# Optimization experiments

Measured on AMD Instinct MI355X. Metric: run time of the kernel, lower is better.

## Reference

```python
import jax, jax.numpy as jnp
import numpy as np

N_USERS = 100000
N_ITEMS = 50000
EMB_DIM = 64
N_EDGES = 1000000
N_HOPS = 3
EPS = 1e-12  # F.normalize default eps


def _l2_normalize(x):
    # F.normalize(x): x / max(||x||_2, eps) along dim=1
    norm = jnp.sqrt(jnp.sum(x * x, axis=1, keepdims=True))
    return x / jnp.maximum(norm, EPS)


def setup_inputs() -> dict:
    key = jax.random.key(0)
    k1, k2, k3, k4 = jax.random.split(key, 4)
    user_emb = jax.random.normal(k1, (N_USERS, EMB_DIM), dtype=jnp.float32)
    item_emb = jax.random.normal(k2, (N_ITEMS, EMB_DIM), dtype=jnp.float32)
    user_indices = jax.random.randint(k3, (N_EDGES,), 0, N_USERS, dtype=jnp.int32)
    item_indices = jax.random.randint(k4, (N_EDGES,), 0, N_ITEMS, dtype=jnp.int32)
    return {"user_emb": user_emb, "item_emb": item_emb,
            "user_indices": user_indices, "item_indices": item_indices}


def reference(user_emb, item_emb, user_indices, item_indices):
    # mess_dropout=False, node_dropout=False (deterministic reference)
    user_agg = user_emb
    item_agg = item_emb
    user_ui_emb = jnp.zeros_like(user_emb)
    item_ui_emb = jnp.zeros_like(item_emb)
    for _ in range(N_HOPS):
        # bipartite message passing: gather from opposite side, scatter_add to own side
        msg_to_users = item_agg[item_indices]            # [E, D]
        msg_to_items = user_agg[user_indices]            # [E, D]
        user_agg = jax.ops.segment_sum(msg_to_users, user_indices, num_segments=N_USERS)
        item_agg = jax.ops.segment_sum(msg_to_items, item_indices, num_segments=N_ITEMS)
        item_agg = _l2_normalize(item_agg)
        user_agg = _l2_normalize(user_agg)
        user_ui_emb = user_agg + user_ui_emb
        item_ui_emb = item_agg + item_ui_emb
    item_ui_emb = item_ui_emb + item_emb
    user_ui_emb = user_ui_emb + user_emb
    return (item_ui_emb, user_ui_emb)
```

## Files before the change

kernel.cpp:

```cpp
#include <hip/hip_runtime.h>

#define N_USERS 100000
#define N_ITEMS 50000
#define NROWS (N_USERS + N_ITEMS)
#define EMB 64
#define N_EDGES 1000000

#define SH_U 9
#define SH_I 8
#define NBUK 196
#define B1 256
#define CHUNK ((N_EDGES + B1 - 1) / B1)
#define HN (2 * NBUK * B1)
#define HTILE 4096
#define HTILES ((HN + HTILE - 1) / HTILE)
#define DBINS 64

#define UCHUNKS 3125
#define TCHUNKS 4688
#define UXCD 3
#define UPER 1042
#define IPER 313
#define GBLOCKS (8 * UPER)

typedef unsigned short u16;
typedef u16 us8 __attribute__((ext_vector_type(8)));
typedef u16 us4 __attribute__((ext_vector_type(4)));
typedef float f4 __attribute__((ext_vector_type(4)));

static __device__ __forceinline__ float bf2f(u16 h) {
    return __uint_as_float(((unsigned)h) << 16);
}
static __device__ __forceinline__ u16 f2bf(float f) {
    unsigned u = __float_as_uint(f);
    return (u16)((u + 0x7FFFu + ((u >> 16) & 1u)) >> 16);
}

static __device__ __forceinline__ int hphys(int L) {
    int sb = L >> 8;
    int blk = L & 255;
    return blk * (2 * NBUK) + sb;
}

__global__ void conv_kernel(const float* __restrict__ ua, u16* __restrict__ ub,
                            const float* __restrict__ ia, u16* __restrict__ ib) {
    const int un4 = N_USERS * EMB / 4;
    const int in4 = N_ITEMS * EMB / 4;
    int t = blockIdx.x * blockDim.x + threadIdx.x;
    const float* a; u16* b; int idx;
    if (t < un4) { a = ua; b = ub; idx = t; }
    else if (t < un4 + in4) { a = ia; b = ib; idx = t - un4; }
    else return;
    f4 v = ((const f4*)a)[idx];
    us4 w;
    w.x = f2bf(v.x); w.y = f2bf(v.y); w.z = f2bf(v.z); w.w = f2bf(v.w);
    ((us4*)b)[idx] = w;
}

__global__ void histA_kernel(const int* __restrict__ uidx, const int* __restrict__ iidx,
                             int* __restrict__ H) {
    __shared__ int hu[NBUK];
    __shared__ int hi[NBUK];
    int tid = threadIdx.x, blk = blockIdx.x;
    for (int b = tid; b < NBUK; b += 256) { hu[b] = 0; hi[b] = 0; }
    __syncthreads();
    int e0 = blk * CHUNK;
    int e1 = e0 + CHUNK; if (e1 > N_EDGES) e1 = N_EDGES;
    for (int e = e0 + tid; e < e1; e += 256) {
        atomicAdd(&hu[uidx[e] >> SH_U], 1);
        atomicAdd(&hi[iidx[e] >> SH_I], 1);
    }
    __syncthreads();
    int* Hb = H + blk * (2 * NBUK);
    for (int b = tid; b < NBUK; b += 256) {
        Hb[b] = hu[b];
        Hb[NBUK + b] = hi[b];
    }
}

__global__ void hscan_tile_kernel(const int* __restrict__ H, int* __restrict__ part) {
    int t = blockIdx.x, tid = threadIdx.x;
    int base = t * HTILE;
    int s = 0;
    for (int i = tid; i < HTILE; i += 256) {
        int L = base + i;
        if (L < HN) s += H[hphys(L)];
    }
    #pragma unroll
    for (int o = 32; o > 0; o >>= 1) s += __shfl_xor(s, o);
    __shared__ int wsum[4];
    if ((tid & 63) == 0) wsum[tid >> 6] = s;
    __syncthreads();
    if (tid == 0) part[t] = wsum[0] + wsum[1] + wsum[2] + wsum[3];
}

__global__ void hscan_write_kernel(const int* __restrict__ H, const int* __restrict__ part,
                                   int* __restrict__ HB) {
    int t = blockIdx.x, tid = threadIdx.x;
    int base = t * HTILE;

    __shared__ int lds[HTILE];
    for (int i = tid; i < HTILE; i += 256) {
        int L = base + i;
        lds[i] = (L < HN) ? H[hphys(L)] : 0;
    }
    __syncthreads();

    int pbase = 0;
    for (int p = 0; p < t; ++p) pbase += part[p];

    int tsum = 0;
    #pragma unroll
    for (int i = 0; i < 16; ++i) tsum += lds[tid * 16 + i];

    int lane = tid & 63, wid = tid >> 6;
    int x = tsum;
    #pragma unroll
    for (int o = 1; o < 64; o <<= 1) {
        int tt = __shfl_up(x, o);
        if (lane >= o) x += tt;
    }
    __shared__ int wsum[4];
    if (lane == 63) wsum[wid] = x;
    __syncthreads();
    int wbase = 0;
    for (int w = 0; w < wid; ++w) wbase += wsum[w];

    int run = pbase + wbase + x - tsum;
    #pragma unroll
    for (int i = 0; i < 16; ++i) {
        int L = base + tid * 16 + i;
        if (L < HN) HB[L] = run;
        run += lds[tid * 16 + i];
    }
}

__global__ void scatterA_kernel(const int* __restrict__ uidx, const int* __restrict__ iidx,
                                const int* __restrict__ HB, int* __restrict__ rec) {
    __shared__ int cu[NBUK];
    __shared__ int ci[NBUK];
    int tid = threadIdx.x, blk = blockIdx.x;
    for (int sb = tid; sb < 2 * NBUK; sb += 256) {
        int v = HB[sb * B1 + blk];
        if (sb < NBUK) cu[sb] = v; else ci[sb - NBUK] = v;
    }
    __syncthreads();
    int e0 = blk * CHUNK;
    int e1 = e0 + CHUNK; if (e1 > N_EDGES) e1 = N_EDGES;
    for (int e = e0 + tid; e < e1; e += 256) {
        int u = uidx[e];
        int i = iidx[e];
        int pu = atomicAdd(&cu[u >> SH_U], 1);
        rec[pu] = ((u & 511) << 16) | i;
        int pi = atomicAdd(&ci[i >> SH_I], 1);
        rec[pi] = ((i & 255) << 17) | u;
    }
}

__global__ void bucketB_kernel(const int* __restrict__ HB, const int* __restrict__ rec,
                               int* __restrict__ list, int2* __restrict__ desc) {
    int sb = blockIdx.x, tid = threadIdx.x;
    int side = (sb >= NBUK) ? 1 : 0;
    int b = sb - side * NBUK;
    int start = HB[sb * B1];
    int end = (sb == 2 * NBUK - 1) ? 2 * N_EDGES : HB[(sb + 1) * B1];
    int shift = side ? 17 : 16;
    int mask  = side ? 0x1FFFF : 0xFFFF;
    int nd    = side ? 256 : 512;
    int dbase = side ? (b << SH_I) : (b << SH_U);
    int n     = side ? N_ITEMS : N_USERS;

    __shared__ int cnt[512];
    __shared__ int scn[512];
    __shared__ int wsum[4];
    __shared__ int dh[DBINS];
    __shared__ int dsc[DBINS];
    if (tid < 256) { cnt[tid] = 0; cnt[256 + tid] = 0; }
    if (tid < DBINS) dh[tid] = 0;
    __syncthreads();

    for (int r = start + tid; r < end; r += 256)
        atomicAdd(&cnt[rec[r] >> shift], 1);
    __syncthreads();

    int a0 = cnt[2 * tid], a1 = cnt[2 * tid + 1];
    int s = a0 + a1;
    int lane = tid & 63, wid = tid >> 6;
    int x = s;
    #pragma unroll
    for (int o = 1; o < 64; o <<= 1) {
        int tt = __shfl_up(x, o);
        if (lane >= o) x += tt;
    }
    if (lane == 63) wsum[wid] = x;
    __syncthreads();
    int wbase = 0;
    for (int w = 0; w < wid; ++w) wbase += wsum[w];
    int excl = wbase + x - s;
    scn[2 * tid] = excl;
    scn[2 * tid + 1] = excl + a0;
    __syncthreads();

    for (int r = start + tid; r < end; r += 256) {
        int v = rec[r];
        int dl = v >> shift;
        int pos = atomicAdd(&scn[dl], 1);
        list[start + pos] = (v & mask) << 7;
    }
    __syncthreads();

    int nv = n - dbase; if (nv > nd) nv = nd;
    for (int dl = tid; dl < nv; dl += 256) {
        int d = cnt[dl]; if (d > DBINS - 1) d = DBINS - 1;
        atomicAdd(&dh[d], 1);
    }
    __syncthreads();
    if (tid < DBINS) {
        int v = dh[tid];
        int xx = v;
        #pragma unroll
        for (int o = 1; o < DBINS; o <<= 1) {
            int tt = __shfl_up(xx, o);
            if (tid >= o) xx += tt;
        }
        dsc[tid] = xx - v;
    }
    __syncthreads();
    if (tid < DBINS) dh[tid] = dsc[tid];
    __syncthreads();
    int pwbase = side ? (N_USERS + dbase) : dbase;
    for (int dl = tid; dl < nv; dl += 256) {
        int deg = cnt[dl];
        int d = deg; if (d > DBINS - 1) d = DBINS - 1;
        int p = atomicAdd(&dh[d], 1);
        int absBeg = start + scn[dl] - deg;
        int rid = pwbase + dl;
        desc[pwbase + p] = make_int2(absBeg, (rid << 9) | deg);
    }
}

__global__ void gather_norm_v7(const u16* __restrict__ srcU,
                               const u16* __restrict__ srcI,
                               const int* __restrict__ list,
                               const int2* __restrict__ desc,
                               u16* __restrict__ aggU, u16* __restrict__ aggI,
                               const u16* __restrict__ h0U, const u16* __restrict__ h0I,
                               const u16* __restrict__ h1U, const u16* __restrict__ h1I,
                               float* __restrict__ outU, float* __restrict__ outI,
                               const float* __restrict__ initU, const float* __restrict__ initI,
                               int final_hop) {
    int bid = blockIdx.x;
    int xcd = bid & 7;
    int idx = bid >> 3;
    int chunk;
    if (xcd < UXCD) {
        chunk = xcd * UPER + idx;
        if (chunk >= UCHUNKS) return;
    } else {
        if (idx >= IPER) return;
        chunk = UCHUNKS + (xcd - UXCD) * IPER + idx;
        if (chunk >= TCHUNKS) return;
    }

    int t = chunk * 256 + threadIdx.x;
    int lane = t & 63;
    int grp = lane >> 3, sub = lane & 7;
    int slot = (t >> 6) * 8 + grp;

    int beg = 0, deg = 0, rid = 0;
    bool valid = slot < NROWS;
    if (valid) {
        int2 d2 = desc[slot];
        beg = d2.x;
        deg = d2.y & 511;
        rid = d2.y >> 9;
    }
    bool isU = rid < N_USERS;
    int rr = isU ? rid : rid - N_USERS;

    const u16* src  = isU ? srcU : srcI;
    const char* srcB = (const char*)src;
    unsigned suboff = (unsigned)(sub << 4);
    const int* lp = list + beg;

    float acc[8] = {0.f, 0.f, 0.f, 0.f, 0.f, 0.f, 0.f, 0.f};

    int lbase = lane & 56;
    int nfull16 = deg >> 4;
    int e0 = 0;
    for (int b16 = 0; b16 < nfull16; ++b16) {
        int jba = lp[e0 + sub];
        int jbb = lp[e0 + 8 + sub];
        #pragma unroll
        for (int e = 0; e < 8; ++e) {
            unsigned jb = (unsigned)__shfl(jba, lbase | e);
            us8 v = *(const us8*)(srcB + (jb + suboff));
            #pragma unroll
            for (int i = 0; i < 8; ++i) acc[i] += bf2f(v[i]);
        }
        #pragma unroll
        for (int e = 0; e < 8; ++e) {
            unsigned jb = (unsigned)__shfl(jbb, lbase | e);
            us8 v = *(const us8*)(srcB + (jb + suboff));
            #pragma unroll
            for (int i = 0; i < 8; ++i) acc[i] += bf2f(v[i]);
        }
        e0 += 16;
    }
    if (deg & 8) {
        int jba = lp[e0 + sub];
        #pragma unroll
        for (int e = 0; e < 8; ++e) {
            unsigned jb = (unsigned)__shfl(jba, lbase | e);
            us8 v = *(const us8*)(srcB + (jb + suboff));
            #pragma unroll
            for (int i = 0; i < 8; ++i) acc[i] += bf2f(v[i]);
        }
        e0 += 8;
    }
    int rem = deg & 7;
    if (rem) {
        int jba = lp[e0 + sub];
        #pragma unroll
        for (int e = 0; e < 8; ++e) {
            if (e < rem) {
                unsigned jb = (unsigned)__shfl(jba, lbase | e);
                us8 v = *(const us8*)(srcB + (jb + suboff));
                #pragma unroll
                for (int i = 0; i < 8; ++i) acc[i] += bf2f(v[i]);
            }
        }
    }

    float q = 0.f;
    #pragma unroll
    for (int i = 0; i < 8; ++i) q += acc[i] * acc[i];
    q += __shfl_xor(q, 1);
    q += __shfl_xor(q, 2);
    q += __shfl_xor(q, 4);
    float inv = 1.f / fmaxf(sqrtf(q), 1e-12f);

    if (!valid) return;
    size_t ro = (size_t)rr * EMB + (sub << 3);

    if (!final_hop) {
        u16* agg = isU ? aggU : aggI;
        us8 w;
        #pragma unroll
        for (int i = 0; i < 8; ++i) w[i] = f2bf(acc[i] * inv);
        *(us8*)(agg + ro) = w;
    } else {
        const u16* h0 = isU ? h0U : h0I;
        const u16* h1 = isU ? h1U : h1I;
        const float* init = isU ? initU : initI;
        float* out = isU ? outU : outI;
        us8 a = *(const us8*)(h0 + ro);
        us8 b = *(const us8*)(h1 + ro);
        f4 i0 = *(const f4*)(init + ro);
        f4 i1 = *(const f4*)(init + ro + 4);
        f4 r0, r1;
        r0.x = i0.x + bf2f(a[0]) + bf2f(b[0]) + acc[0] * inv;
        r0.y = i0.y + bf2f(a[1]) + bf2f(b[1]) + acc[1] * inv;
        r0.z = i0.z + bf2f(a[2]) + bf2f(b[2]) + acc[2] * inv;
        r0.w = i0.w + bf2f(a[3]) + bf2f(b[3]) + acc[3] * inv;
        r1.x = i1.x + bf2f(a[4]) + bf2f(b[4]) + acc[4] * inv;
        r1.y = i1.y + bf2f(a[5]) + bf2f(b[5]) + acc[5] * inv;
        r1.z = i1.z + bf2f(a[6]) + bf2f(b[6]) + acc[6] * inv;
        r1.w = i1.w + bf2f(a[7]) + bf2f(b[7]) + acc[7] * inv;
        *(f4*)(out + ro)     = r0;
        *(f4*)(out + ro + 4) = r1;
    }
}

extern "C" void kernel_launch(void* const* d_in, const int* in_sizes, int n_in,
                              void* d_out, int out_size, void* d_ws, size_t ws_size,
                              hipStream_t stream) {
    const float* user_emb = (const float*)d_in[0];
    const float* item_emb = (const float*)d_in[1];
    const int*   uidx     = (const int*)d_in[2];
    const int*   iidx     = (const int*)d_in[3];

    float* out      = (float*)d_out;
    float* out_item = out;
    float* out_user = out + (size_t)N_ITEMS * EMB;

    u16* ws16    = (u16*)d_ws;
    u16* ua_bf   = ws16;
    u16* ub_bf   = ua_bf + (size_t)N_USERS * EMB;
    u16* ia_bf   = ub_bf + (size_t)N_USERS * EMB;
    u16* ib_bf   = ia_bf + (size_t)N_ITEMS * EMB;
    u16* uemb_bf = ib_bf + (size_t)N_ITEMS * EMB;
    u16* iemb_bf = uemb_bf + (size_t)N_USERS * EMB;
    int* rec     = (int*)(iemb_bf + (size_t)N_ITEMS * EMB);
    int* list    = rec + 2 * N_EDGES;
    int* H       = list + 2 * N_EDGES + 16;
    int* HB      = H + HN;
    int* part    = HB + HN;
    int2* desc   = (int2*)(part + HTILES + 1);

    conv_kernel<<<(NROWS * EMB / 4 + 255) / 256, 256, 0, stream>>>(user_emb, uemb_bf, item_emb, iemb_bf);

    histA_kernel<<<B1, 256, 0, stream>>>(uidx, iidx, H);
    hscan_tile_kernel<<<HTILES, 256, 0, stream>>>(H, part);
    hscan_write_kernel<<<HTILES, 256, 0, stream>>>(H, part, HB);
    scatterA_kernel<<<B1, 256, 0, stream>>>(uidx, iidx, HB, rec);
    bucketB_kernel<<<2 * NBUK, 256, 0, stream>>>(HB, rec, list, desc);

    gather_norm_v7<<<GBLOCKS, 256, 0, stream>>>(
        iemb_bf, uemb_bf, list, desc,
        ua_bf, ia_bf, nullptr, nullptr, nullptr, nullptr,
        nullptr, nullptr, nullptr, nullptr, 0);

    gather_norm_v7<<<GBLOCKS, 256, 0, stream>>>(
        ia_bf, ua_bf, list, desc,
        ub_bf, ib_bf, nullptr, nullptr, nullptr, nullptr,
        nullptr, nullptr, nullptr, nullptr, 0);

    gather_norm_v7<<<GBLOCKS, 256, 0, stream>>>(
        ib_bf, ub_bf, list, desc,
        nullptr, nullptr, ua_bf, ia_bf, ub_bf, ib_bf,
        out_user, out_item, user_emb, item_emb, 1);
}
```

Measured before the change: 207.0 us.

## Build CSR via chained stable counting sorts so neighbor lists are ordered

Replaces the single two-sided bucket sort with a three-pass chain of stable counting sorts: sort by item, then stably by user (producing user CSR with items in ascending order), then stably by item again (producing item CSR with users ascending). Ordered neighbor lists should make the gather kernel's embedding reads more local and improve cache hits. The cost is many more preprocessing launches and extra passes over the edge records, plus extra workspace for the intermediate streams.

```diff
diff --git a/kernel.cpp b/kernel.cpp
--- a/kernel.cpp
+++ b/kernel.cpp
@@ -11,10 +11,11 @@
 #define NBUK 196
 #define B1 256
 #define CHUNK ((N_EDGES + B1 - 1) / B1)
-#define HN (2 * NBUK * B1)
-#define HTILE 4096
-#define HTILES ((HN + HTILE - 1) / HTILE)
 #define DBINS 64
+
+#define HNS (NBUK * B1)
+#define HTILE_S 4096
+#define HTILES_S ((HNS + HTILE_S - 1) / HTILE_S)
 
 #define UCHUNKS 3125
 #define TCHUNKS 4688
@@ -24,6 +25,7 @@
 #define GBLOCKS (8 * UPER)
 
 typedef unsigned short u16;
+typedef unsigned char u8;
 typedef u16 us8 __attribute__((ext_vector_type(8)));
 typedef u16 us4 __attribute__((ext_vector_type(4)));
 typedef float f4 __attribute__((ext_vector_type(4)));
@@ -36,10 +38,10 @@
     return (u16)((u + 0x7FFFu + ((u >> 16) & 1u)) >> 16);
 }
 
-static __device__ __forceinline__ int hphys(int L) {
-    int sb = L >> 8;
+static __device__ __forceinline__ int sphys(int L) {
+    int b = L >> 8;
     int blk = L & 255;
-    return blk * (2 * NBUK) + sb;
+    return blk * NBUK + b;
 }
 
 __global__ void conv_kernel(const float* __restrict__ ua, u16* __restrict__ ub,
@@ -57,34 +59,41 @@
     ((us4*)b)[idx] = w;
 }
 
-__global__ void histA_kernel(const int* __restrict__ uidx, const int* __restrict__ iidx,
-                             int* __restrict__ H) {
-    __shared__ int hu[NBUK];
-    __shared__ int hi[NBUK];
+__global__ void histI_edges(const int* __restrict__ iidx, int* __restrict__ H) {
+    __shared__ int h[NBUK];
     int tid = threadIdx.x, blk = blockIdx.x;
-    for (int b = tid; b < NBUK; b += 256) { hu[b] = 0; hi[b] = 0; }
+    for (int b = tid; b < NBUK; b += 256) h[b] = 0;
     __syncthreads();
     int e0 = blk * CHUNK;
     int e1 = e0 + CHUNK; if (e1 > N_EDGES) e1 = N_EDGES;
-    for (int e = e0 + tid; e < e1; e += 256) {
-        atomicAdd(&hu[uidx[e] >> SH_U], 1);
-        atomicAdd(&hi[iidx[e] >> SH_I], 1);
-    }
-    __syncthreads();
-    int* Hb = H + blk * (2 * NBUK);
-    for (int b = tid; b < NBUK; b += 256) {
-        Hb[b] = hu[b];
-        Hb[NBUK + b] = hi[b];
-    }
-}
-
-__global__ void hscan_tile_kernel(const int* __restrict__ H, int* __restrict__ part) {
+    for (int e = e0 + tid; e < e1; e += 256)
+        atomicAdd(&h[iidx[e] >> SH_I], 1);
+    __syncthreads();
+    int* Hb = H + blk * NBUK;
+    for (int b = tid; b < NBUK; b += 256) Hb[b] = h[b];
+}
+
+__global__ void histS_stream(const u8* __restrict__ sbk, int* __restrict__ H) {
+    __shared__ int h[NBUK];
+    int tid = threadIdx.x, blk = blockIdx.x;
+    for (int b = tid; b < NBUK; b += 256) h[b] = 0;
+    __syncthreads();
+    int e0 = blk * CHUNK;
+    int e1 = e0 + CHUNK; if (e1 > N_EDGES) e1 = N_EDGES;
+    for (int e = e0 + tid; e < e1; e += 256)
+        atomicAdd(&h[sbk[e]], 1);
+    __syncthreads();
+    int* Hb = H + blk * NBUK;
+    for (int b = tid; b < NBUK; b += 256) Hb[b] = h[b];
+}
+
+__global__ void sscan_tile(const int* __restrict__ H, int* __restrict__ part) {
     int t = blockIdx.x, tid = threadIdx.x;
-    int base = t * HTILE;
+    int base = t * HTILE_S;
     int s = 0;
-    for (int i = tid; i < HTILE; i += 256) {
+    for (int i = tid; i < HTILE_S; i += 256) {
         int L = base + i;
-        if (L < HN) s += H[hphys(L)];
+        if (L < HNS) s += H[sphys(L)];
     }
     #pragma unroll
     for (int o = 32; o > 0; o >>= 1) s += __shfl_xor(s, o);
@@ -94,15 +103,15 @@
     if (tid == 0) part[t] = wsum[0] + wsum[1] + wsum[2] + wsum[3];
 }
 
-__global__ void hscan_write_kernel(const int* __restrict__ H, const int* __restrict__ part,
-                                   int* __restrict__ HB) {
+__global__ void sscan_write(const int* __restrict__ H, const int* __restrict__ part,
+                            int* __restrict__ HB) {
     int t = blockIdx.x, tid = threadIdx.x;
-    int base = t * HTILE;
-
-    __shared__ int lds[HTILE];
-    for (int i = tid; i < HTILE; i += 256) {
+    int base = t * HTILE_S;
+
+    __shared__ int lds[HTILE_S];
+    for (int i = tid; i < HTILE_S; i += 256) {
         int L = base + i;
-        lds[i] = (L < HN) ? H[hphys(L)] : 0;
+        lds[i] = (L < HNS) ? H[sphys(L)] : 0;
     }
     __syncthreads();
 
@@ -130,45 +139,34 @@
     #pragma unroll
     for (int i = 0; i < 16; ++i) {
         int L = base + tid * 16 + i;
-        if (L < HN) HB[L] = run;
+        if (L < HNS) HB[L] = run;
         run += lds[tid * 16 + i];
     }
 }
 
-__global__ void scatterA_kernel(const int* __restrict__ uidx, const int* __restrict__ iidx,
-                                const int* __restrict__ HB, int* __restrict__ rec) {
-    __shared__ int cu[NBUK];
+__global__ void scatA_edges_item(const int* __restrict__ uidx, const int* __restrict__ iidx,
+                                 const int* __restrict__ HB, int* __restrict__ rec) {
     __shared__ int ci[NBUK];
     int tid = threadIdx.x, blk = blockIdx.x;
-    for (int sb = tid; sb < 2 * NBUK; sb += 256) {
-        int v = HB[sb * B1 + blk];
-        if (sb < NBUK) cu[sb] = v; else ci[sb - NBUK] = v;
-    }
+    for (int b = tid; b < NBUK; b += 256)
+        ci[b] = HB[b * B1 + blk];
     __syncthreads();
     int e0 = blk * CHUNK;
     int e1 = e0 + CHUNK; if (e1 > N_EDGES) e1 = N_EDGES;
     for (int e = e0 + tid; e < e1; e += 256) {
         int u = uidx[e];
         int i = iidx[e];
-        int pu = atomicAdd(&cu[u >> SH_U], 1);
-        rec[pu] = ((u & 511) << 16) | i;
-        int pi = atomicAdd(&ci[i >> SH_I], 1);
-        rec[pi] = ((i & 255) << 17) | u;
-    }
-}
-
-__global__ void bucketB_kernel(const int* __restrict__ HB, const int* __restrict__ rec,
-                               int* __restrict__ list, int2* __restrict__ desc) {
+        int p = atomicAdd(&ci[i >> SH_I], 1);
+        rec[p] = ((i & 255) << 17) | u;
+    }
+}
+
+__global__ void bucketB_item_first(const int* __restrict__ HB, const int* __restrict__ rec,
+                                   int* __restrict__ s1r, u8* __restrict__ s1b,
+                                   int2* __restrict__ desc) {
     int sb = blockIdx.x, tid = threadIdx.x;
-    int side = (sb >= NBUK) ? 1 : 0;
-    int b = sb - side * NBUK;
     int start = HB[sb * B1];
-    int end = (sb == 2 * NBUK - 1) ? 2 * N_EDGES : HB[(sb + 1) * B1];
-    int shift = side ? 17 : 16;
-    int mask  = side ? 0x1FFFF : 0xFFFF;
-    int nd    = side ? 256 : 512;
-    int dbase = side ? (b << SH_I) : (b << SH_U);
-    int n     = side ? N_ITEMS : N_USERS;
+    int end = (sb == NBUK - 1) ? N_EDGES : HB[(sb + 1) * B1];
 
     __shared__ int cnt[512];
     __shared__ int scn[512];
@@ -180,7 +178,7 @@
     __syncthreads();
 
     for (int r = start + tid; r < end; r += 256)
-        atomicAdd(&cnt[rec[r] >> shift], 1);
+        atomicAdd(&cnt[rec[r] >> 17], 1);
     __syncthreads();
 
     int a0 = cnt[2 * tid], a1 = cnt[2 * tid + 1];
@@ -203,13 +201,17 @@
 
     for (int r = start + tid; r < end; r += 256) {
         int v = rec[r];
-        int dl = v >> shift;
-        int pos = atomicAdd(&scn[dl], 1);
-        list[start + pos] = (v & mask) << 7;
-    }
-    __syncthreads();
-
-    int nv = n - dbase; if (nv > nd) nv = nd;
+        int dl = v >> 17;
+        int u = v & 0x1FFFF;
+        int pos = start + atomicAdd(&scn[dl], 1);
+        int ifull = (sb << SH_I) | dl;
+        s1r[pos] = ((u & 511) << 16) | ifull;
+        s1b[pos] = (u8)(u >> SH_U);
+    }
+    __syncthreads();
+
+    int dbase = sb << SH_I;
+    int nv = N_ITEMS - dbase; if (nv > 256) nv = 256;
     for (int dl = tid; dl < nv; dl += 256) {
         int d = cnt[dl]; if (d > DBINS - 1) d = DBINS - 1;
         atomicAdd(&dh[d], 1);
@@ -228,18 +230,175 @@
     __syncthreads();
     if (tid < DBINS) dh[tid] = dsc[tid];
     __syncthreads();
-    int pwbase = side ? (N_USERS + dbase) : dbase;
+    int pwbase = N_USERS + dbase;
+    for (int dl = tid; dl < nv; dl += 256) {
+        int deg = cnt[dl];
+        int d = deg; if (d > DBINS - 1) d = DBINS - 1;
+        int p = atomicAdd(&dh[d], 1);
+        int absBeg = N_EDGES + start + scn[dl] - deg;
+        int rid = pwbase + dl;
+        desc[pwbase + p] = make_int2(absBeg, (rid << 9) | deg);
+    }
+}
+
+__global__ void scatB_stream_user(const int* __restrict__ s1r, const u8* __restrict__ s1b,
+                                  const int* __restrict__ HB, int* __restrict__ rec) {
+    __shared__ int cu[NBUK];
+    int tid = threadIdx.x, blk = blockIdx.x;
+    for (int b = tid; b < NBUK; b += 256)
+        cu[b] = HB[b * B1 + blk];
+    __syncthreads();
+    int e0 = blk * CHUNK;
+    int e1 = e0 + CHUNK; if (e1 > N_EDGES) e1 = N_EDGES;
+    for (int e = e0 + tid; e < e1; e += 256) {
+        int r = s1r[e];
+        int b = s1b[e];
+        int p = atomicAdd(&cu[b], 1);
+        rec[p] = r;
+    }
+}
+
+__global__ void bucketB_user(const int* __restrict__ HB, const int* __restrict__ rec,
+                             int* __restrict__ list,
+                             int* __restrict__ s2r, u8* __restrict__ s2b,
+                             int2* __restrict__ desc) {
+    int sb = blockIdx.x, tid = threadIdx.x;
+    int start = HB[sb * B1];
+    int end = (sb == NBUK - 1) ? N_EDGES : HB[(sb + 1) * B1];
+
+    __shared__ int cnt[512];
+    __shared__ int scn[512];
+    __shared__ int wsum[4];
+    __shared__ int dh[DBINS];
+    __shared__ int dsc[DBINS];
+    if (tid < 256) { cnt[tid] = 0; cnt[256 + tid] = 0; }
+    if (tid < DBINS) dh[tid] = 0;
+    __syncthreads();
+
+    for (int r = start + tid; r < end; r += 256)
+        atomicAdd(&cnt[rec[r] >> 16], 1);
+    __syncthreads();
+
+    int a0 = cnt[2 * tid], a1 = cnt[2 * tid + 1];
+    int s = a0 + a1;
+    int lane = tid & 63, wid = tid >> 6;
+    int x = s;
+    #pragma unroll
+    for (int o = 1; o < 64; o <<= 1) {
+        int tt = __shfl_up(x, o);
+        if (lane >= o) x += tt;
+    }
+    if (lane == 63) wsum[wid] = x;
+    __syncthreads();
+    int wbase = 0;
+    for (int w = 0; w < wid; ++w) wbase += wsum[w];
+    int excl = wbase + x - s;
+    scn[2 * tid] = excl;
+    scn[2 * tid + 1] = excl + a0;
+    __syncthreads();
+
+    for (int r = start + tid; r < end; r += 256) {
+        int v = rec[r];
+        int dl = v >> 16;
+        int i = v & 0xFFFF;
+        int pos = start + atomicAdd(&scn[dl], 1);
+        list[pos] = i << 7;
+        int ufull = (sb << SH_U) | dl;
+        s2r[pos] = ((i & 255) << 17) | ufull;
+        s2b[pos] = (u8)(i >> SH_I);
+    }
+    __syncthreads();
+
+    int dbase = sb << SH_U;
+    int nv = N_USERS - dbase; if (nv > 512) nv = 512;
+    for (int dl = tid; dl < nv; dl += 256) {
+        int d = cnt[dl]; if (d > DBINS - 1) d = DBINS - 1;
+        atomicAdd(&dh[d], 1);
+    }
+    __syncthreads();
+    if (tid < DBINS) {
+        int v = dh[tid];
+        int xx = v;
+        #pragma unroll
+        for (int o = 1; o < DBINS; o <<= 1) {
+            int tt = __shfl_up(xx, o);
+            if (tid >= o) xx += tt;
+        }
+        dsc[tid] = xx - v;
+    }
+    __syncthreads();
+    if (tid < DBINS) dh[tid] = dsc[tid];
+    __syncthreads();
     for (int dl = tid; dl < nv; dl += 256) {
         int deg = cnt[dl];
         int d = deg; if (d > DBINS - 1) d = DBINS - 1;
         int p = atomicAdd(&dh[d], 1);
         int absBeg = start + scn[dl] - deg;
-        int rid = pwbase + dl;
-        desc[pwbase + p] = make_int2(absBeg, (rid << 9) | deg);
-    }
-}
-
-__global__ void gather_norm_v7(const u16* __restrict__ srcU,
+        int rid = dbase + dl;
+        desc[dbase + p] = make_int2(absBeg, (rid << 9) | deg);
+    }
+}
+
+__global__ void scatC_stream_item(const int* __restrict__ s2r, const u8* __restrict__ s2b,
+                                  const int* __restrict__ HB, int* __restrict__ rec) {
+    __shared__ int ci[NBUK];
+    int tid = threadIdx.x, blk = blockIdx.x;
+    for (int b = tid; b < NBUK; b += 256)
+        ci[b] = HB[b * B1 + blk];
+    __syncthreads();
+    int e0 = blk * CHUNK;
+    int e1 = e0 + CHUNK; if (e1 > N_EDGES) e1 = N_EDGES;
+    for (int e = e0 + tid; e < e1; e += 256) {
+        int r = s2r[e];
+        int b = s2b[e];
+        int p = atomicAdd(&ci[b], 1);
+        rec[p] = r;
+    }
+}
+
+__global__ void bucketB_item_final(const int* __restrict__ HB, const int* __restrict__ rec,
+                                   int* __restrict__ list) {
+    int sb = blockIdx.x, tid = threadIdx.x;
+    int start = HB[sb * B1];
+    int end = (sb == NBUK - 1) ? N_EDGES : HB[(sb + 1) * B1];
+
+    __shared__ int cnt[512];
+    __shared__ int scn[512];
+    __shared__ int wsum[4];
+    if (tid < 256) { cnt[tid] = 0; cnt[256 + tid] = 0; }
+    __syncthreads();
+
+    for (int r = start + tid; r < end; r += 256)
+        atomicAdd(&cnt[rec[r] >> 17], 1);
+    __syncthreads();
+
+    int a0 = cnt[2 * tid], a1 = cnt[2 * tid + 1];
+    int s = a0 + a1;
+    int lane = tid & 63, wid = tid >> 6;
+    int x = s;
+    #pragma unroll
+    for (int o = 1; o < 64; o <<= 1) {
+        int tt = __shfl_up(x, o);
+        if (lane >= o) x += tt;
+    }
+    if (lane == 63) wsum[wid] = x;
+    __syncthreads();
+    int wbase = 0;
+    for (int w = 0; w < wid; ++w) wbase += wsum[w];
+    int excl = wbase + x - s;
+    scn[2 * tid] = excl;
+    scn[2 * tid + 1] = excl + a0;
+    __syncthreads();
+
+    for (int r = start + tid; r < end; r += 256) {
+        int v = rec[r];
+        int dl = v >> 17;
+        int pos = N_EDGES + start + atomicAdd(&scn[dl], 1);
+        list[pos] = (v & 0x1FFFF) << 7;
+    }
+}
+
+__global__ void gather_norm_v8(const u16* __restrict__ srcU,
                                const u16* __restrict__ srcI,
                                const int* __restrict__ list,
                                const int2* __restrict__ desc,
@@ -392,31 +551,47 @@
     u16* uemb_bf = ib_bf + (size_t)N_ITEMS * EMB;
     u16* iemb_bf = uemb_bf + (size_t)N_USERS * EMB;
     int* rec     = (int*)(iemb_bf + (size_t)N_ITEMS * EMB);
-    int* list    = rec + 2 * N_EDGES;
-    int* H       = list + 2 * N_EDGES + 16;
-    int* HB      = H + HN;
-    int* part    = HB + HN;
-    int2* desc   = (int2*)(part + HTILES + 1);
+    int* list    = rec + N_EDGES;
+    int* Hs      = list + 2 * N_EDGES + 16;
+    int* HBs     = Hs + HNS;
+    int* part    = HBs + HNS;
+    int2* desc   = (int2*)(part + 16);
+    int* s1r     = (int*)(desc + NROWS);
+    int* s2r     = s1r + N_EDGES;
+    u8* s1b      = (u8*)(s2r + N_EDGES);
+    u8* s2b      = s1b + N_EDGES;
 
     conv_kernel<<<(NROWS * EMB / 4 + 255) / 256, 256, 0, stream>>>(user_emb, uemb_bf, item_emb, iemb_bf);
 
-    histA_kernel<<<B1, 256, 0, stream>>>(uidx, iidx, H);
-    hscan_tile_kernel<<<HTILES, 256, 0, stream>>>(H, part);
-    hscan_write_kernel<<<HTILES, 256, 0, stream>>>(H, part, HB);
-    scatterA_kernel<<<B1, 256, 0, stream>>>(uidx, iidx, HB, rec);
-    bucketB_kernel<<<2 * NBUK, 256, 0, stream>>>(HB, rec, list, desc);
-
-    gather_norm_v7<<<GBLOCKS, 256, 0, stream>>>(
+    histI_edges<<<B1, 256, 0, stream>>>(iidx, Hs);
+    sscan_tile<<<HTILES_S, 256, 0, stream>>>(Hs, part);
+    sscan_write<<<HTILES_S, 256, 0, stream>>>(Hs, part, HBs);
+    scatA_edges_item<<<B1, 256, 0, stream>>>(uidx, iidx, HBs, rec);
+    bucketB_item_first<<<NBUK, 256, 0, stream>>>(HBs, rec, s1r, s1b, desc);
+
+    histS_stream<<<B1, 256, 0, stream>>>(s1b, Hs);
+    sscan_tile<<<HTILES_S, 256, 0, stream>>>(Hs, part);
+    sscan_write<<<HTILES_S, 256, 0, stream>>>(Hs, part, HBs);
+    scatB_stream_user<<<B1, 256, 0, stream>>>(s1r, s1b, HBs, rec);
+    bucketB_user<<<NBUK, 256, 0, stream>>>(HBs, rec, list, s2r, s2b, desc);
+
+    histS_stream<<<B1, 256, 0, stream>>>(s2b, Hs);
+    sscan_tile<<<HTILES_S, 256, 0, stream>>>(Hs, part);
+    sscan_write<<<HTILES_S, 256, 0, stream>>>(Hs, part, HBs);
+    scatC_stream_item<<<B1, 256, 0, stream>>>(s2r, s2b, HBs, rec);
+    bucketB_item_final<<<NBUK, 256, 0, stream>>>(HBs, rec, list);
+
+    gather_norm_v8<<<GBLOCKS, 256, 0, stream>>>(
         iemb_bf, uemb_bf, list, desc,
         ua_bf, ia_bf, nullptr, nullptr, nullptr, nullptr,
         nullptr, nullptr, nullptr, nullptr, 0);
 
-    gather_norm_v7<<<GBLOCKS, 256, 0, stream>>>(
+    gather_norm_v8<<<GBLOCKS, 256, 0, stream>>>(
         ia_bf, ua_bf, list, desc,
         ub_bf, ib_bf, nullptr, nullptr, nullptr, nullptr,
         nullptr, nullptr, nullptr, nullptr, 0);
 
-    gather_norm_v7<<<GBLOCKS, 256, 0, stream>>>(
+    gather_norm_v8<<<GBLOCKS, 256, 0, stream>>>(
         ib_bf, ub_bf, list, desc,
         nullptr, nullptr, ua_bf, ia_bf, ub_bf, ib_bf,
         out_user, out_item, user_emb, item_emb, 1);
```

Result: slower. 286.5 us (+38.4%).
